# Performance work log

Measured on AMD Instinct MI355X. Metric: run time of the kernel, lower is better.

## Reference

```python
import jax, jax.numpy as jnp
import numpy as np

SUBSTEPS = 4  # fixed dopri5 substeps per output interval
S0, I0, R0 = 0.99, 0.01, 0.0


def _dopri5_step(f, y, dt):
    # Classic Dormand-Prince 5(4) tableau; 5th-order solution needs stages 1,3,4,5,6.
    k1 = f(y)
    k2 = f(y + dt * (1.0 / 5.0) * k1)
    k3 = f(y + dt * (3.0 / 40.0 * k1 + 9.0 / 40.0 * k2))
    k4 = f(y + dt * (44.0 / 45.0 * k1 - 56.0 / 15.0 * k2 + 32.0 / 9.0 * k3))
    k5 = f(y + dt * (19372.0 / 6561.0 * k1 - 25360.0 / 2187.0 * k2
                     + 64448.0 / 6561.0 * k3 - 212.0 / 729.0 * k4))
    k6 = f(y + dt * (9017.0 / 3168.0 * k1 - 355.0 / 33.0 * k2
                     + 46732.0 / 5247.0 * k3 + 49.0 / 176.0 * k4
                     - 5103.0 / 18656.0 * k5))
    return y + dt * (35.0 / 384.0 * k1 + 500.0 / 1113.0 * k3
                     + 125.0 / 192.0 * k4 - 2187.0 / 6784.0 * k5
                     + 11.0 / 84.0 * k6)


def _solve_sir(beta, gamma, t):
    def f(y):
        S, I, R = y[0], y[1], y[2]
        dS = -beta * S * I
        dI = beta * S * I - gamma * I
        dR = gamma * I
        return jnp.stack([dS, dI, dR])

    y0 = jnp.array([S0, I0, R0], dtype=jnp.float32)
    dts = jnp.diff(t)  # [T-1]

    def interval(y, dt):
        h = dt / SUBSTEPS
        def sub(y, _):
            return _dopri5_step(f, y, h), None
        y, _ = jax.lax.scan(sub, y, None, length=SUBSTEPS)
        return y, y

    _, ys = jax.lax.scan(interval, y0, dts)
    return jnp.concatenate([y0[None, :], ys], axis=0)  # [T, 3]


def setup_inputs() -> dict:
    key = jax.random.key(0)
    ks = jax.random.split(key, 14)
    D_IN, D_OUT, T = 8192, 8192, 8192
    s = 0.02
    inp = {
        "x": jax.random.normal(ks[0], (1, D_IN), dtype=jnp.float32),
        "t": jnp.arange(T, dtype=jnp.float32) * (10.0 / T),
        # Encoder: D_IN -> 128 -> 64 -> 2
        "enc_w1": jax.random.normal(ks[1], (D_IN, 128), dtype=jnp.float32) * s,
        "enc_b1": jnp.zeros((128,), dtype=jnp.float32),
        "enc_w2": jax.random.normal(ks[2], (128, 64), dtype=jnp.float32) * s,
        "enc_b2": jnp.zeros((64,), dtype=jnp.float32),
        "enc_w3": jax.random.normal(ks[3], (64, 2), dtype=jnp.float32) * s,
        "enc_b3": jnp.zeros((2,), dtype=jnp.float32),
        # Decoder: 3 -> 64 -> 128 -> D_OUT
        "dec_w1": jax.random.normal(ks[4], (3, 64), dtype=jnp.float32) * s,
        "dec_b1": jnp.zeros((64,), dtype=jnp.float32),
        "dec_w2": jax.random.normal(ks[5], (64, 128), dtype=jnp.float32) * s,
        "dec_b2": jnp.zeros((128,), dtype=jnp.float32),
        "dec_w3": jax.random.normal(ks[6], (128, D_OUT), dtype=jnp.float32) * s,
        "dec_b3": jnp.zeros((D_OUT,), dtype=jnp.float32),
    }
    return inp


def reference(x, t, enc_w1, enc_b1, enc_w2, enc_b2, enc_w3, enc_b3,
              dec_w1, dec_b1, dec_w2, dec_b2, dec_w3, dec_b3):
    # Encoder (batch=1, matching the original's scalar-unbind SIR semantics)
    h = jax.nn.relu(x @ enc_w1 + enc_b1)
    h = jax.nn.relu(h @ enc_w2 + enc_b2)
    p = h @ enc_w3 + enc_b3            # [1, 2]
    beta, gamma = p[0, 0], p[0, 1]

    sol = _solve_sir(beta, gamma, t)   # [T, 3]

    # Decoder
    h = jax.nn.relu(sol @ dec_w1 + dec_b1)
    h = jax.nn.relu(h @ dec_w2 + dec_b2)
    out = jax.nn.relu(h @ dec_w3 + dec_b3)  # [T, D_OUT]
    return out
```

## Files before the change

### kernel.cpp

```cpp
#include <hip/hip_runtime.h>
#include <math.h>
#include <stdint.h>


typedef __attribute__((ext_vector_type(8))) short short8_t;
typedef __attribute__((ext_vector_type(4))) float f32x4;

#define DT_C 0.001220703125f

__device__ __forceinline__ unsigned short f2bf_rn(float f) {
  unsigned int u = __float_as_uint(f);
  unsigned int r = (u + 0x7fffu + ((u >> 16) & 1u)) >> 16;
  return (unsigned short)r;
}
__device__ __forceinline__ float bf2f(unsigned short h) {
  return __uint_as_float(((unsigned int)h) << 16);
}

__device__ __forceinline__ void gl2lds16(const void* g, void* lds_base) {
  __builtin_amdgcn_global_load_lds(
      (const __attribute__((address_space(1))) unsigned int*)(uintptr_t)g,
      (__attribute__((address_space(3))) unsigned int*)(uintptr_t)lds_base,
      16, 0, 0);
}


__device__ __forceinline__ void f_sir(float beta, float gamma,
                                      const float y[3], float d[3]) {
  float SI = y[0] * y[1];
  d[0] = -beta * SI;
  d[1] = beta * SI - gamma * y[1];
  d[2] = gamma * y[1];
}

__device__ __forceinline__ void dopri5_step(float beta, float gamma,
                                            float y[3], float dt) {
  float k1[3], k2[3], k3[3], k4[3], k5[3], k6[3], tmp[3];
  f_sir(beta, gamma, y, k1);
#pragma unroll
  for (int c = 0; c < 3; ++c)
    tmp[c] = y[c] + dt * (0.2f * k1[c]);
  f_sir(beta, gamma, tmp, k2);
#pragma unroll
  for (int c = 0; c < 3; ++c)
    tmp[c] = y[c] + dt * (0.075f * k1[c] + 0.225f * k2[c]);
  f_sir(beta, gamma, tmp, k3);
#pragma unroll
  for (int c = 0; c < 3; ++c)
    tmp[c] = y[c] + dt * ((44.0f / 45.0f) * k1[c] + (-56.0f / 15.0f) * k2[c] +
                          (32.0f / 9.0f) * k3[c]);
  f_sir(beta, gamma, tmp, k4);
#pragma unroll
  for (int c = 0; c < 3; ++c)
    tmp[c] = y[c] + dt * ((19372.0f / 6561.0f) * k1[c] +
                          (-25360.0f / 2187.0f) * k2[c] +
                          (64448.0f / 6561.0f) * k3[c] +
                          (-212.0f / 729.0f) * k4[c]);
  f_sir(beta, gamma, tmp, k5);
#pragma unroll
  for (int c = 0; c < 3; ++c)
    tmp[c] = y[c] + dt * ((9017.0f / 3168.0f) * k1[c] +
                          (-355.0f / 33.0f) * k2[c] +
                          (46732.0f / 5247.0f) * k3[c] +
                          (49.0f / 176.0f) * k4[c] +
                          (-5103.0f / 18656.0f) * k5[c]);
  f_sir(beta, gamma, tmp, k6);
#pragma unroll
  for (int c = 0; c < 3; ++c)
    y[c] = y[c] + dt * ((35.0f / 384.0f) * k1[c] +
                        (500.0f / 1113.0f) * k3[c] +
                        (125.0f / 192.0f) * k4[c] +
                        (-2187.0f / 6784.0f) * k5[c] +
                        (11.0f / 84.0f) * k6[c]);
}

__global__ __launch_bounds__(256) void pre_kernel(
    const float* __restrict__ x, const float* __restrict__ w1,
    float* __restrict__ partial,
    const float* __restrict__ w3, unsigned short* __restrict__ Wt) {
  __shared__ __align__(16) float smem[128 * 65];
  int tid = threadIdx.x;
  if (blockIdx.x < 64) {
    float4* sh = (float4*)smem;
    int j4 = tid & 31, kh = tid >> 5;
    int kbase = blockIdx.x * 128 + kh * 16;
    float4 a; a.x = 0.f; a.y = 0.f; a.z = 0.f; a.w = 0.f;
#pragma unroll
    for (int r = 0; r < 16; ++r) {
      int k = kbase + r;
      float xv = x[k];
      float4 wv = *(const float4*)(w1 + (size_t)k * 128 + j4 * 4);
      a.x = fmaf(xv, wv.x, a.x);
      a.y = fmaf(xv, wv.y, a.y);
      a.z = fmaf(xv, wv.z, a.z);
      a.w = fmaf(xv, wv.w, a.w);
    }
    sh[tid] = a;
    __syncthreads();
    if (tid < 32) {
      float4 s = sh[tid];
#pragma unroll
      for (int h = 1; h < 8; ++h) {
        float4 o = sh[h * 32 + tid];
        s.x += o.x; s.y += o.y; s.z += o.z; s.w += o.w;
      }
      *(float4*)(partial + blockIdx.x * 128 + tid * 4) = s;
    }
  } else {
    float* tl = smem;
    int n0 = (blockIdx.x - 64) * 64;
#pragma unroll
    for (int e = 0; e < 32; ++e) {
      int idx = e * 256 + tid;
      int k = idx >> 6, c = idx & 63;
      tl[k * 65 + c] = w3[(size_t)k * 8192 + n0 + c];
    }
    __syncthreads();
    int nl = tid >> 2, q = tid & 3;
#pragma unroll
    for (int w = 0; w < 4; ++w) {
      int k0 = q * 32 + w * 8;
      short8_t vh, vl;
#pragma unroll
      for (int jj = 0; jj < 8; ++jj) {
        float v = tl[(k0 + jj) * 65 + nl];
        unsigned short h = f2bf_rn(v);
        vh[jj] = (short)h;
        vl[jj] = (short)f2bf_rn(v - bf2f(h));
      }
      *(short8_t*)(Wt + (size_t)(n0 + nl) * 256 + k0) = vh;
      *(short8_t*)(Wt + (size_t)(n0 + nl) * 256 + 128 + k0) = vl;
    }
  }
}

__global__ __launch_bounds__(256) void prep_kernel(
    const float* __restrict__ partial, const float* __restrict__ b1,
    const float* __restrict__ w2, const float* __restrict__ b2,
    const float* __restrict__ w3, const float* __restrict__ b3,
    float* __restrict__ bg, float* __restrict__ ys) {
  __shared__ float h1s[128];
  __shared__ float h2s[64];
  __shared__ float bgs[2];
  __shared__ float Y0[16][3];
  __shared__ float Y1[256][3];
  int t = threadIdx.x;
  if (t < 128) {
    float s = b1[t];
    for (int b = 0; b < 64; ++b) s += partial[b * 128 + t];
    h1s[t] = fmaxf(s, 0.0f);
  }
  __syncthreads();
  if (t < 64) {
    float a = b2[t];
    for (int k = 0; k < 128; ++k) a = fmaf(h1s[k], w2[k * 64 + t], a);
    h2s[t] = fmaxf(a, 0.0f);
  }
  __syncthreads();
  if (t < 2) {
    float p = b3[t];
    for (int k = 0; k < 64; ++k) p = fmaf(h2s[k], w3[k * 2 + t], p);
    bgs[t] = p;
    bg[t] = p;
  }
  __syncthreads();
  float beta = bgs[0], gamma = bgs[1];
  if (t == 0) {
    float y[3] = {0.99f, 0.01f, 0.0f};
    Y0[0][0] = y[0]; Y0[0][1] = y[1]; Y0[0][2] = y[2];
    for (int j = 1; j < 16; ++j) {
      dopri5_step(beta, gamma, y, 512.0f * DT_C);
      Y0[j][0] = y[0]; Y0[j][1] = y[1]; Y0[j][2] = y[2];
    }
  }
  __syncthreads();
  if (t < 16) {
    float y[3] = {Y0[t][0], Y0[t][1], Y0[t][2]};
    Y1[t * 16][0] = y[0]; Y1[t * 16][1] = y[1]; Y1[t * 16][2] = y[2];
    for (int s = 1; s < 16; ++s) {
      dopri5_step(beta, gamma, y, 32.0f * DT_C);
      Y1[t * 16 + s][0] = y[0]; Y1[t * 16 + s][1] = y[1]; Y1[t * 16 + s][2] = y[2];
    }
  }
  __syncthreads();
  {
    float y[3] = {Y1[t][0], Y1[t][1], Y1[t][2]};
    ys[(t * 8) * 3 + 0] = y[0]; ys[(t * 8) * 3 + 1] = y[1]; ys[(t * 8) * 3 + 2] = y[2];
    for (int s = 1; s < 8; ++s) {
      dopri5_step(beta, gamma, y, 4.0f * DT_C);
      ys[(t * 8 + s) * 3 + 0] = y[0];
      ys[(t * 8 + s) * 3 + 1] = y[1];
      ys[(t * 8 + s) * 3 + 2] = y[2];
    }
  }
}

__global__ __launch_bounds__(256) void dec12f_kernel(
    const float* __restrict__ bg, const float* __restrict__ ys,
    const float* __restrict__ w1, const float* __restrict__ b1,
    const float* __restrict__ w2, const float* __restrict__ b2,
    unsigned short* __restrict__ Apack) {
  __shared__ float sols[128 * 4];
  __shared__ float w1s[192];
  __shared__ float b1s[64];
  __shared__ float b2s[128];
  __shared__ float h1s[128 * 66];
  int tid = threadIdx.x;
  int i0 = blockIdx.x * 128;
  if (tid < 192) w1s[tid] = w1[tid];
  if (tid < 64) b1s[tid] = b1[tid];
  if (tid < 128) b2s[tid] = b2[tid];
  if (tid < 33) {
    const float h = 0.25f * DT_C;
    float beta = bg[0], gamma = bg[1];
    int w = blockIdx.x * 32 + tid - 1;
    if (w < 0) {
      sols[0] = 0.99f; sols[1] = 0.01f; sols[2] = 0.0f;
    } else {
      float y[3] = {ys[w * 3 + 0], ys[w * 3 + 1], ys[w * 3 + 2]};
#pragma unroll
      for (int iv = 0; iv < 4; ++iv) {
        dopri5_step(beta, gamma, y, h);
        dopri5_step(beta, gamma, y, h);
        dopri5_step(beta, gamma, y, h);
        dopri5_step(beta, gamma, y, h);
        int local = 4 * w + iv + 1 - i0;
        if (local >= 0 && local < 128) {
          sols[local * 4 + 0] = y[0];
          sols[local * 4 + 1] = y[1];
          sols[local * 4 + 2] = y[2];
        }
      }
    }
  }
  __syncthreads();
#pragma unroll
  for (int e = 0; e < 32; ++e) {
    int idx = e * 256 + tid;
    int i = idx >> 6, j = idx & 63;
    float v = b1s[j];
    v = fmaf(sols[i * 4 + 0], w1s[j], v);
    v = fmaf(sols[i * 4 + 1], w1s[64 + j], v);
    v = fmaf(sols[i * 4 + 2], w1s[128 + j], v);
    h1s[i * 66 + j] = fmaxf(v, 0.0f);
  }
  __syncthreads();
  int tx = tid & 15, ty = tid >> 4;
  float acc[8][8];
#pragma unroll
  for (int a = 0; a < 8; ++a)
#pragma unroll
    for (int b = 0; b < 8; ++b) acc[a][b] = 0.0f;
  for (int j = 0; j < 64; ++j) {
    float a[8];
#pragma unroll
    for (int mm = 0; mm < 8; ++mm) a[mm] = h1s[(ty * 8 + mm) * 66 + j];
    float4 q0 = *(const float4*)(w2 + j * 128 + tx * 8);
    float4 q1 = *(const float4*)(w2 + j * 128 + tx * 8 + 4);
    float b[8] = {q0.x, q0.y, q0.z, q0.w, q1.x, q1.y, q1.z, q1.w};
#pragma unroll
    for (int mm = 0; mm < 8; ++mm)
#pragma unroll
      for (int nn = 0; nn < 8; ++nn)
        acc[mm][nn] = fmaf(a[mm], b[nn], acc[mm][nn]);
  }
#pragma unroll
  for (int mm = 0; mm < 8; ++mm) {
    int row = i0 + ty * 8 + mm;
    short8_t vh, vl;
#pragma unroll
    for (int nn = 0; nn < 8; ++nn) {
      float v = fmaxf(acc[mm][nn] + b2s[tx * 8 + nn], 0.0f);
      unsigned short h = f2bf_rn(v);
      vh[nn] = (short)h;
      vl[nn] = (short)f2bf_rn(v - bf2f(h));
    }
    *(short8_t*)(Apack + (size_t)row * 256 + tx * 8) = vh;
    *(short8_t*)(Apack + (size_t)row * 256 + 128 + tx * 8) = vl;
  }
}

__global__ __launch_bounds__(256) void gemm_bf16_kernel(
    const unsigned short* __restrict__ A, const unsigned short* __restrict__ B,
    const float* __restrict__ bias, float* __restrict__ out) {
  __shared__ unsigned short Ah[128 * 32];
  __shared__ unsigned short Al[128 * 32];
  __shared__ unsigned short Bh[128 * 32];
  __shared__ unsigned short Bl[128 * 32];
  int tid = threadIdx.x;
  int bid = blockIdx.x;
  int swz = (bid & 7) * 512 + (bid >> 3);
  int by = swz & 63, bx = swz >> 6;
  int m0 = by * 128;
  int n0 = bx * 128;
  int lane = tid & 63, wave = tid >> 6;
  int wm = (wave >> 1) * 64, wn = (wave & 1) * 64;
  int lrow = lane & 15, lgrp = lane >> 4;
  int lr4 = lane >> 2, lp = lane & 3;

  f32x4 acc[4][4];
  f32x4 z = {0.0f, 0.0f, 0.0f, 0.0f};
#pragma unroll
  for (int mi = 0; mi < 4; ++mi)
#pragma unroll
    for (int ni = 0; ni < 4; ++ni) acc[mi][ni] = z;

  for (int c = 0; c < 4; ++c) {
    int kin = c * 32;
#pragma unroll
    for (int i = 0; i < 2; ++i) {
      int seg = wave * 2 + i;
      int r = seg * 16 + lr4;
      int g = lp ^ (r & 3);
      const unsigned short* ar = A + (size_t)(m0 + r) * 256 + kin + g * 8;
      const unsigned short* br = B + (size_t)(n0 + r) * 256 + kin + g * 8;
      gl2lds16(ar, &Ah[seg * 512]);
      gl2lds16(ar + 128, &Al[seg * 512]);
      gl2lds16(br, &Bh[seg * 512]);
      gl2lds16(br + 128, &Bl[seg * 512]);
    }
    __syncthreads();

    short8_t ah[4], bh[4];
#pragma unroll
    for (int mi = 0; mi < 4; ++mi) {
      int r = wm + mi * 16 + lrow;
      int p = lgrp ^ (r & 3);
      ah[mi] = *(const short8_t*)(&Ah[r * 32 + p * 8]);
    }
#pragma unroll
    for (int ni = 0; ni < 4; ++ni) {
      int r = wn + ni * 16 + lrow;
      int p = lgrp ^ (r & 3);
      bh[ni] = *(const short8_t*)(&Bh[r * 32 + p * 8]);
    }
#pragma unroll
    for (int mi = 0; mi < 4; ++mi)
#pragma unroll
      for (int ni = 0; ni < 4; ++ni)
        acc[mi][ni] = __builtin_amdgcn_mfma_f32_16x16x32_bf16(
            ah[mi], bh[ni], acc[mi][ni], 0, 0, 0);
    {
      short8_t bl[4];
#pragma unroll
      for (int ni = 0; ni < 4; ++ni) {
        int r = wn + ni * 16 + lrow;
        int p = lgrp ^ (r & 3);
        bl[ni] = *(const short8_t*)(&Bl[r * 32 + p * 8]);
      }
#pragma unroll
      for (int mi = 0; mi < 4; ++mi)
#pragma unroll
        for (int ni = 0; ni < 4; ++ni)
          acc[mi][ni] = __builtin_amdgcn_mfma_f32_16x16x32_bf16(
              ah[mi], bl[ni], acc[mi][ni], 0, 0, 0);
    }
    {
      short8_t al[4];
#pragma unroll
      for (int mi = 0; mi < 4; ++mi) {
        int r = wm + mi * 16 + lrow;
        int p = lgrp ^ (r & 3);
        al[mi] = *(const short8_t*)(&Al[r * 32 + p * 8]);
      }
#pragma unroll
      for (int mi = 0; mi < 4; ++mi)
#pragma unroll
        for (int ni = 0; ni < 4; ++ni)
          acc[mi][ni] = __builtin_amdgcn_mfma_f32_16x16x32_bf16(
              al[mi], bh[ni], acc[mi][ni], 0, 0, 0);
    }
    __syncthreads();
  }

  float bv[4];
#pragma unroll
  for (int ni = 0; ni < 4; ++ni) bv[ni] = bias[n0 + wn + ni * 16 + lrow];
#pragma unroll
  for (int mi = 0; mi < 4; ++mi)
#pragma unroll
    for (int ni = 0; ni < 4; ++ni) {
      int col = n0 + wn + ni * 16 + lrow;
#pragma unroll
      for (int r = 0; r < 4; ++r) {
        int row = m0 + wm + mi * 16 + lgrp * 4 + r;
        out[(size_t)row * 8192 + col] = fmaxf(acc[mi][ni][r] + bv[ni], 0.0f);
      }
    }
}


extern "C" void kernel_launch(void* const* d_in, const int* in_sizes, int n_in,
                              void* d_out, int out_size, void* d_ws, size_t ws_size,
                              hipStream_t stream) {
  const float* x      = (const float*)d_in[0];
  const float* enc_w1 = (const float*)d_in[2];
  const float* enc_b1 = (const float*)d_in[3];
  const float* enc_w2 = (const float*)d_in[4];
  const float* enc_b2 = (const float*)d_in[5];
  const float* enc_w3 = (const float*)d_in[6];
  const float* enc_b3 = (const float*)d_in[7];
  const float* dec_w1 = (const float*)d_in[8];
  const float* dec_b1 = (const float*)d_in[9];
  const float* dec_w2 = (const float*)d_in[10];
  const float* dec_b2 = (const float*)d_in[11];
  const float* dec_w3 = (const float*)d_in[12];
  const float* dec_b3 = (const float*)d_in[13];
  float* out = (float*)d_out;

  float* ws      = (float*)d_ws;
  float* bg      = ws;
  float* partial = ws + 64;
  float* ys      = ws + 8320;
  unsigned short* Apack = (unsigned short*)((char*)d_ws + 65536);
  unsigned short* Wt    = (unsigned short*)((char*)d_ws + 65536 + 4194304);

  hipLaunchKernelGGL(pre_kernel, dim3(192), dim3(256), 0, stream,
                     x, enc_w1, partial, dec_w3, Wt);
  hipLaunchKernelGGL(prep_kernel, dim3(1), dim3(256), 0, stream,
                     partial, enc_b1, enc_w2, enc_b2, enc_w3, enc_b3, bg, ys);
  hipLaunchKernelGGL(dec12f_kernel, dim3(64), dim3(256), 0, stream,
                     bg, ys, dec_w1, dec_b1, dec_w2, dec_b2, Apack);
  hipLaunchKernelGGL(gemm_bf16_kernel, dim3(4096), dim3(256), 0, stream,
                     Apack, Wt, dec_b3, out);
}
```

Baseline: 393.9 us.

## Enlarge GEMM tiles to 256x256 with 512 threads and double-buffered LDS

The decoder's bf16 split-precision GEMM tile grows from 128x128 to 256x256, using 8 waves that each own a 128x64 sub-tile, and the grid shrinks from 4096 to 1024 blocks. LDS staging is double-buffered, so the next K-chunk's global-to-LDS loads are issued while the current chunk feeds the MFMAs, and one barrier per iteration is dropped. The goal is less redundant A/B traffic and hidden load latency. In exchange, accumulator register pressure rises (128 accumulator floats per lane) alongside a launch-bounds hint of 2 blocks per CU. That risks spills, and 128KB of LDS per block limits occupancy to one block per CU.

```diff
diff --git a/kernel.cpp b/kernel.cpp
--- a/kernel.cpp
+++ b/kernel.cpp
@@ -280,32 +280,32 @@
   }
 }
 
-__global__ __launch_bounds__(256) void gemm_bf16_kernel(
+__global__ __launch_bounds__(512, 2) void gemm_bf16_kernel(
     const unsigned short* __restrict__ A, const unsigned short* __restrict__ B,
     const float* __restrict__ bias, float* __restrict__ out) {
-  __shared__ unsigned short Ah[128 * 32];
-  __shared__ unsigned short Al[128 * 32];
-  __shared__ unsigned short Bh[128 * 32];
-  __shared__ unsigned short Bl[128 * 32];
+  __shared__ unsigned short Ah[2][256 * 32];
+  __shared__ unsigned short Al[2][256 * 32];
+  __shared__ unsigned short Bh[2][256 * 32];
+  __shared__ unsigned short Bl[2][256 * 32];
   int tid = threadIdx.x;
   int bid = blockIdx.x;
-  int swz = (bid & 7) * 512 + (bid >> 3);
-  int by = swz & 63, bx = swz >> 6;
-  int m0 = by * 128;
-  int n0 = bx * 128;
+  int swz = (bid & 7) * 128 + (bid >> 3);
+  int by = swz & 31, bx = swz >> 5;
+  int m0 = by * 256;
+  int n0 = bx * 256;
   int lane = tid & 63, wave = tid >> 6;
-  int wm = (wave >> 1) * 64, wn = (wave & 1) * 64;
+  int wm = (wave >> 2) * 128, wn = (wave & 3) * 64;
   int lrow = lane & 15, lgrp = lane >> 4;
   int lr4 = lane >> 2, lp = lane & 3;
 
-  f32x4 acc[4][4];
+  f32x4 acc[8][4];
   f32x4 z = {0.0f, 0.0f, 0.0f, 0.0f};
 #pragma unroll
-  for (int mi = 0; mi < 4; ++mi)
+  for (int mi = 0; mi < 8; ++mi)
 #pragma unroll
     for (int ni = 0; ni < 4; ++ni) acc[mi][ni] = z;
 
-  for (int c = 0; c < 4; ++c) {
+  auto STAGE = [&](int buf, int c) {
     int kin = c * 32;
 #pragma unroll
     for (int i = 0; i < 2; ++i) {
@@ -314,28 +314,36 @@
       int g = lp ^ (r & 3);
       const unsigned short* ar = A + (size_t)(m0 + r) * 256 + kin + g * 8;
       const unsigned short* br = B + (size_t)(n0 + r) * 256 + kin + g * 8;
-      gl2lds16(ar, &Ah[seg * 512]);
-      gl2lds16(ar + 128, &Al[seg * 512]);
-      gl2lds16(br, &Bh[seg * 512]);
-      gl2lds16(br + 128, &Bl[seg * 512]);
-    }
-    __syncthreads();
-
-    short8_t ah[4], bh[4];
-#pragma unroll
-    for (int mi = 0; mi < 4; ++mi) {
+      gl2lds16(ar,       &Ah[buf][seg * 512]);
+      gl2lds16(ar + 128, &Al[buf][seg * 512]);
+      gl2lds16(br,       &Bh[buf][seg * 512]);
+      gl2lds16(br + 128, &Bl[buf][seg * 512]);
+    }
+  };
+
+  STAGE(0, 0);
+  __syncthreads();
+
+#pragma unroll
+  for (int c = 0; c < 4; ++c) {
+    int cur = c & 1;
+    if (c < 3) STAGE(cur ^ 1, c + 1);
+
+    short8_t ah[8], bh[4];
+#pragma unroll
+    for (int mi = 0; mi < 8; ++mi) {
       int r = wm + mi * 16 + lrow;
       int p = lgrp ^ (r & 3);
-      ah[mi] = *(const short8_t*)(&Ah[r * 32 + p * 8]);
+      ah[mi] = *(const short8_t*)(&Ah[cur][r * 32 + p * 8]);
     }
 #pragma unroll
     for (int ni = 0; ni < 4; ++ni) {
       int r = wn + ni * 16 + lrow;
       int p = lgrp ^ (r & 3);
-      bh[ni] = *(const short8_t*)(&Bh[r * 32 + p * 8]);
-    }
-#pragma unroll
-    for (int mi = 0; mi < 4; ++mi)
+      bh[ni] = *(const short8_t*)(&Bh[cur][r * 32 + p * 8]);
+    }
+#pragma unroll
+    for (int mi = 0; mi < 8; ++mi)
 #pragma unroll
       for (int ni = 0; ni < 4; ++ni)
         acc[mi][ni] = __builtin_amdgcn_mfma_f32_16x16x32_bf16(
@@ -346,38 +354,38 @@
       for (int ni = 0; ni < 4; ++ni) {
         int r = wn + ni * 16 + lrow;
         int p = lgrp ^ (r & 3);
-        bl[ni] = *(const short8_t*)(&Bl[r * 32 + p * 8]);
-      }
-#pragma unroll
-      for (int mi = 0; mi < 4; ++mi)
+        bl[ni] = *(const short8_t*)(&Bl[cur][r * 32 + p * 8]);
+      }
+#pragma unroll
+      for (int mi = 0; mi < 8; ++mi)
 #pragma unroll
         for (int ni = 0; ni < 4; ++ni)
           acc[mi][ni] = __builtin_amdgcn_mfma_f32_16x16x32_bf16(
               ah[mi], bl[ni], acc[mi][ni], 0, 0, 0);
     }
     {
-      short8_t al[4];
-#pragma unroll
-      for (int mi = 0; mi < 4; ++mi) {
+      short8_t al[8];
+#pragma unroll
+      for (int mi = 0; mi < 8; ++mi) {
         int r = wm + mi * 16 + lrow;
         int p = lgrp ^ (r & 3);
-        al[mi] = *(const short8_t*)(&Al[r * 32 + p * 8]);
-      }
-#pragma unroll
-      for (int mi = 0; mi < 4; ++mi)
+        al[mi] = *(const short8_t*)(&Al[cur][r * 32 + p * 8]);
+      }
+#pragma unroll
+      for (int mi = 0; mi < 8; ++mi)
 #pragma unroll
         for (int ni = 0; ni < 4; ++ni)
           acc[mi][ni] = __builtin_amdgcn_mfma_f32_16x16x32_bf16(
               al[mi], bh[ni], acc[mi][ni], 0, 0, 0);
     }
-    __syncthreads();
+    if (c < 3) __syncthreads();
   }
 
   float bv[4];
 #pragma unroll
   for (int ni = 0; ni < 4; ++ni) bv[ni] = bias[n0 + wn + ni * 16 + lrow];
 #pragma unroll
-  for (int mi = 0; mi < 4; ++mi)
+  for (int mi = 0; mi < 8; ++mi)
 #pragma unroll
     for (int ni = 0; ni < 4; ++ni) {
       int col = n0 + wn + ni * 16 + lrow;
@@ -421,6 +429,6 @@
                      partial, enc_b1, enc_w2, enc_b2, enc_w3, enc_b3, bg, ys);
   hipLaunchKernelGGL(dec12f_kernel, dim3(64), dim3(256), 0, stream,
                      bg, ys, dec_w1, dec_b1, dec_w2, dec_b2, Apack);
-  hipLaunchKernelGGL(gemm_bf16_kernel, dim3(4096), dim3(256), 0, stream,
+  hipLaunchKernelGGL(gemm_bf16_kernel, dim3(1024), dim3(512), 0, stream,
                      Apack, Wt, dec_b3, out);
 }
```

Result: faster. 383.3 us (-2.7%).
